# Optimization experiments

Hardware: AMD Instinct MI355X
Metric: run time of the kernel (lower is better)

## Reference

```python
import jax, jax.numpy as jnp
import numpy as np

N = 50000       # nodes
E = 1_600_000   # edges
F_IN, H1, H2, T, C = 16, 64, 64, 8, 10


def setup_inputs() -> dict:
    key = jax.random.key(0)
    ks = jax.random.split(key, 12)
    def w(k, shp):
        fan_in = shp[0]
        return jax.random.normal(k, shp, dtype=jnp.float32) * (1.0 / np.sqrt(fan_in))
    return {
        "x": jax.random.normal(ks[0], (N, F_IN, T), dtype=jnp.float32),
        "edge_index": jax.random.randint(ks[1], (2, E), 0, N, dtype=jnp.int64),
        "edge_weight": jax.random.uniform(ks[2], (E,), dtype=jnp.float32),
        "W1": w(ks[3], (F_IN, H1)), "b1": jnp.zeros((H1,), jnp.float32),
        "W2": w(ks[4], (H1, H2)),   "b2": jnp.zeros((H2,), jnp.float32),
        "W3": w(ks[5], (H2, H2)),   "b3": jnp.zeros((H2,), jnp.float32),
        "Wseq": w(ks[6], (H2 * T, H2)), "bseq": jnp.zeros((H2,), jnp.float32),
        "Wcls": w(ks[7], (H2, C)),  "bcls": jnp.zeros((C,), jnp.float32),
    }


def reference(x, edge_index, edge_weight, W1, b1, W2, b2, W3, b3, Wseq, bseq, Wcls, bcls):
    n = x.shape[0]
    src, dst = edge_index[0], edge_index[1]
    # GCN: add self-loops with weight 1, symmetric degree normalization
    loops = jnp.arange(n, dtype=src.dtype)
    src_a = jnp.concatenate([src, loops])
    dst_a = jnp.concatenate([dst, loops])
    w_a = jnp.concatenate([edge_weight, jnp.ones((n,), edge_weight.dtype)])
    deg = jax.ops.segment_sum(w_a, dst_a, num_segments=n)
    dinv = jnp.where(deg > 0, jax.lax.rsqrt(jnp.where(deg > 0, deg, 1.0)), 0.0)
    norm = dinv[src_a] * w_a * dinv[dst_a]  # [E+N]

    def conv(h, W, b):
        h = h @ W                                  # [N, out]
        msg = h[src_a] * norm[:, None]             # gather + scale
        return jax.ops.segment_sum(msg, dst_a, num_segments=n) + b

    def per_t(xt):  # xt: [N, F_IN]
        h = jax.nn.relu(conv(xt, W1, b1))
        h = jax.nn.relu(conv(h, W2, b2))
        h = jax.nn.relu(conv(h, W3, b3))
        return h  # [N, H2]

    hs = jax.vmap(per_t)(jnp.moveaxis(x, -1, 0))   # [T, N, H2]
    seq = jnp.transpose(hs, (1, 0, 2)).reshape(n, -1)  # [N, T*H2], t-major like torch.cat
    h = jax.nn.relu(seq @ Wseq + bseq)
    return h @ Wcls + bcls  # [N, C]
```

## Files before the change

kernel.cpp:

```cpp
#include <hip/hip_runtime.h>
#include <hip/hip_fp16.h>

constexpr int N  = 50000;
constexpr int E  = 1600000;
constexpr int T  = 8;
constexpr int H  = 64;
constexpr int C  = 10;

__global__ void deg_count_kernel(const int* __restrict__ ei, const float* __restrict__ w,
                                 float* __restrict__ deg, int* __restrict__ counts) {
  int e = blockIdx.x * blockDim.x + threadIdx.x;
  if (e >= E) return;
  int d = ei[E + e];
  atomicAdd(&deg[d], w[e]);
  atomicAdd(&counts[d], 1);
}

__global__ void dinv_kernel(float* deg) {
  int n = blockIdx.x * blockDim.x + threadIdx.x;
  if (n >= N) return;
  deg[n] = rsqrtf(deg[n] + 1.0f);
}

__global__ void scanA_kernel(const int* __restrict__ counts, int* __restrict__ rowptr,
                             int* __restrict__ bsum) {
  __shared__ int ws[4];
  int b = blockIdx.x, t = threadIdx.x;
  int base = b * 1024 + t * 4;
  int v0 = (base + 0 < N) ? counts[base + 0] : 0;
  int v1 = (base + 1 < N) ? counts[base + 1] : 0;
  int v2 = (base + 2 < N) ? counts[base + 2] : 0;
  int v3 = (base + 3 < N) ? counts[base + 3] : 0;
  int s = v0 + v1 + v2 + v3;
  int lane = t & 63, wid = t >> 6;
  int x = s;
  #pragma unroll
  for (int off = 1; off < 64; off <<= 1) {
    int y = __shfl_up(x, off, 64);
    if (lane >= off) x += y;
  }
  if (lane == 63) ws[wid] = x;
  __syncthreads();
  int woff = 0;
  #pragma unroll
  for (int k = 0; k < 4; ++k) if (k < wid) woff += ws[k];
  int excl = x + woff - s;
  int a = excl;
  a += v0; if (base + 0 < N) rowptr[base + 1] = a;
  a += v1; if (base + 1 < N) rowptr[base + 2] = a;
  a += v2; if (base + 2 < N) rowptr[base + 3] = a;
  a += v3; if (base + 3 < N) rowptr[base + 4] = a;
  if (t == 255) bsum[b] = x + woff;
}

__global__ void scanB_kernel(const int* __restrict__ bsum, int* __restrict__ boff, int nb) {
  int t = threadIdx.x;
  int v = (t < nb) ? bsum[t] : 0;
  int x = v;
  #pragma unroll
  for (int off = 1; off < 64; off <<= 1) {
    int y = __shfl_up(x, off, 64);
    if (t >= off) x += y;
  }
  if (t < nb) boff[t] = x - v;
}

__global__ void scanC_kernel(int* __restrict__ rowptr, const int* __restrict__ boff) {
  int i = blockIdx.x * 256 + threadIdx.x;
  if (i == 0) rowptr[0] = 0;
  if (i < N) rowptr[i + 1] += boff[i >> 10];
}

__global__ void fill_kernel(const int* __restrict__ ei, const float* __restrict__ w,
                            const float* __restrict__ dinv, const int* __restrict__ rowptr,
                            int* __restrict__ fill, int* __restrict__ csr_src,
                            float* __restrict__ csr_norm) {
  int e = blockIdx.x * blockDim.x + threadIdx.x;
  if (e >= E) return;
  int s = ei[e], d = ei[E + e];
  int pos = rowptr[d] + atomicAdd(&fill[d], 1);
  csr_src[pos] = s;
  csr_norm[pos] = dinv[s] * w[e] * dinv[d];
}

__global__ void cvt_x_kernel(const float* __restrict__ x, __half* __restrict__ xh) {
  int i = blockIdx.x * blockDim.x + threadIdx.x;
  if (i >= N * 32) return;
  float4 v = ((const float4*)x)[i];
  __half2 h0; h0.x = __float2half_rn(v.x); h0.y = __float2half_rn(v.y);
  __half2 h1; h1.x = __float2half_rn(v.z); h1.y = __float2half_rn(v.w);
  uint2 u;
  u.x = __builtin_bit_cast(unsigned int, h0);
  u.y = __builtin_bit_cast(unsigned int, h1);
  ((uint2*)xh)[i] = u;
}

__device__ __forceinline__ void accum8(float* acc, uint4 r, float wgt) {
  float2 f0 = __half22float2(__builtin_bit_cast(__half2, r.x));
  float2 f1 = __half22float2(__builtin_bit_cast(__half2, r.y));
  float2 f2 = __half22float2(__builtin_bit_cast(__half2, r.z));
  float2 f3 = __half22float2(__builtin_bit_cast(__half2, r.w));
  acc[0] = fmaf(wgt, f0.x, acc[0]); acc[1] = fmaf(wgt, f0.y, acc[1]);
  acc[2] = fmaf(wgt, f1.x, acc[2]); acc[3] = fmaf(wgt, f1.y, acc[3]);
  acc[4] = fmaf(wgt, f2.x, acc[4]); acc[5] = fmaf(wgt, f2.y, acc[5]);
  acc[6] = fmaf(wgt, f3.x, acc[6]); acc[7] = fmaf(wgt, f3.y, acc[7]);
}

__global__ void agg_x_kernel(const __half* __restrict__ xh, const float* __restrict__ dinv,
                             const int* __restrict__ rowptr, const int* __restrict__ csr_src,
                             const float* __restrict__ csr_norm, float* __restrict__ xagg) {
  int tid = threadIdx.x;
  int w = tid >> 6, l = tid & 63;
  int sub = l >> 4, q = l & 15;
  int n = blockIdx.x * 4 + w;
  float di = dinv[n], dd = di * di;
  int e0 = rowptr[n], e1 = rowptr[n + 1];
  int cnt = e1 - e0 + 1;
  float acc[8] = {0, 0, 0, 0, 0, 0, 0, 0};
  int sA, sB; float wA, wB;
  auto meta = [&](int idx, int& s_, float& w_) {
    if (idx == 0)       { s_ = n; w_ = dd; }
    else if (idx < cnt) { s_ = csr_src[e0 + idx - 1]; w_ = csr_norm[e0 + idx - 1]; }
    else                { s_ = n; w_ = 0.f; }
  };
  meta(sub,     sA, wA);
  meta(sub + 4, sB, wB);
  for (int i = sub; i < cnt; i += 8) {
    uint4 rA = *reinterpret_cast<const uint4*>(xh + (size_t)sA * 128 + q * 8);
    uint4 rB = *reinterpret_cast<const uint4*>(xh + (size_t)sB * 128 + q * 8);
    float uA = wA, uB = wB;
    meta(i + 8,  sA, wA);
    meta(i + 12, sB, wB);
    accum8(acc, rA, uA);
    accum8(acc, rB, uB);
  }
  #pragma unroll
  for (int v = 0; v < 8; ++v) {
    acc[v] += __shfl_xor(acc[v], 16, 64);
    acc[v] += __shfl_xor(acc[v], 32, 64);
  }
  if (sub == 0) {
    float4 o0; o0.x = acc[0]; o0.y = acc[1]; o0.z = acc[2]; o0.w = acc[3];
    float4 o1; o1.x = acc[4]; o1.y = acc[5]; o1.z = acc[6]; o1.w = acc[7];
    float4* dst = (float4*)(xagg + (size_t)n * 128 + q * 8);
    dst[0] = o0; dst[1] = o1;
  }
}

__global__ void dense12_kernel(const float* __restrict__ xagg, const float* __restrict__ W1,
                               const float* __restrict__ b1, const float* __restrict__ W2,
                               __half* __restrict__ G2h) {
  __shared__ float xs[4 * 128];
  __shared__ float h1s[4][8][64];
  int tid = threadIdx.x;
  int n0 = blockIdx.x * 4;
  ((float2*)xs)[tid] = ((const float2*)(xagg + (size_t)n0 * 128))[tid];
  __syncthreads();
  int nb = tid >> 6, j = tid & 63;
  float a[8];
  float bj = b1[j];
  #pragma unroll
  for (int t = 0; t < 8; ++t) a[t] = bj;
  for (int f = 0; f < 16; ++f) {
    float wv = W1[f * 64 + j];
    #pragma unroll
    for (int t = 0; t < 8; ++t) a[t] = fmaf(xs[nb * 128 + f * 8 + t], wv, a[t]);
  }
  #pragma unroll
  for (int t = 0; t < 8; ++t) h1s[nb][t][j] = fmaxf(a[t], 0.f);
  __syncthreads();
  float g[8];
  #pragma unroll
  for (int t = 0; t < 8; ++t) g[t] = 0.f;
  for (int k = 0; k < 64; ++k) {
    float wv = W2[k * 64 + j];
    #pragma unroll
    for (int t = 0; t < 8; ++t) g[t] = fmaf(h1s[nb][t][k], wv, g[t]);
  }
  __half* gp = G2h + (size_t)(n0 + nb) * 512 + j;
  #pragma unroll
  for (int t = 0; t < 8; ++t) gp[t * 64] = __float2half_rn(g[t]);
}

__global__ void conv2w_kernel(const __half* __restrict__ G2h, const float* __restrict__ dinv,
                              const int* __restrict__ rowptr, const int* __restrict__ csr_src,
                              const float* __restrict__ csr_norm, const float* __restrict__ b2,
                              const float* __restrict__ W3, __half* __restrict__ G3h) {
  __shared__ float h2s[4][512];
  int tid = threadIdx.x;
  int w = tid >> 6, l = tid & 63;
  int n0 = blockIdx.x * 4;
  int n = n0 + w;
  float di = dinv[n], dd = di * di;
  int e0 = rowptr[n], e1 = rowptr[n + 1];
  int cnt = e1 - e0 + 1;
  float acc[8] = {0, 0, 0, 0, 0, 0, 0, 0};
  int sm[4]; float wm[4];
  #pragma unroll
  for (int q = 0; q < 4; ++q) {
    int idx = q;
    if (idx == 0)       { sm[q] = n; wm[q] = dd; }
    else if (idx < cnt) { int e = e0 + idx - 1; sm[q] = csr_src[e]; wm[q] = csr_norm[e]; }
    else                { sm[q] = n; wm[q] = 0.f; }
  }
  for (int i = 0; i < cnt; i += 4) {
    uint4 r0 = *reinterpret_cast<const uint4*>(G2h + (size_t)sm[0] * 512 + l * 8);
    uint4 r1 = *reinterpret_cast<const uint4*>(G2h + (size_t)sm[1] * 512 + l * 8);
    uint4 r2 = *reinterpret_cast<const uint4*>(G2h + (size_t)sm[2] * 512 + l * 8);
    uint4 r3 = *reinterpret_cast<const uint4*>(G2h + (size_t)sm[3] * 512 + l * 8);
    float w0 = wm[0], w1 = wm[1], w2 = wm[2], w3 = wm[3];
    #pragma unroll
    for (int q = 0; q < 4; ++q) {
      int idx = i + 4 + q;
      if (idx < cnt) { int e = e0 + idx - 1; sm[q] = csr_src[e]; wm[q] = csr_norm[e]; }
      else           { sm[q] = n; wm[q] = 0.f; }
    }
    accum8(acc, r0, w0);
    accum8(acc, r1, w1);
    accum8(acc, r2, w2);
    accum8(acc, r3, w3);
  }
  #pragma unroll
  for (int q = 0; q < 8; ++q)
    h2s[w][l * 8 + q] = fmaxf(acc[q] + b2[(l * 8 + q) & 63], 0.f);
  __syncthreads();
  int t = tid >> 5;
  int jh = tid & 31, j0 = 2 * jh;
  float g[4][2];
  #pragma unroll
  for (int q = 0; q < 4; ++q) { g[q][0] = 0.f; g[q][1] = 0.f; }
  const float2* W3v = (const float2*)W3;
  for (int k = 0; k < 64; ++k) {
    float2 wv = W3v[k * 32 + jh];
    #pragma unroll
    for (int q = 0; q < 4; ++q) {
      float h = h2s[q][t * 64 + k];
      g[q][0] = fmaf(h, wv.x, g[q][0]);
      g[q][1] = fmaf(h, wv.y, g[q][1]);
    }
  }
  #pragma unroll
  for (int q = 0; q < 4; ++q) {
    __half2 hv;
    hv.x = __float2half_rn(g[q][0]);
    hv.y = __float2half_rn(g[q][1]);
    *reinterpret_cast<__half2*>(G3h + (size_t)(n0 + q) * 512 + t * 64 + j0) = hv;
  }
}

__global__ void conv3w_kernel(const __half* __restrict__ G3h, const float* __restrict__ dinv,
                              const int* __restrict__ rowptr, const int* __restrict__ csr_src,
                              const float* __restrict__ csr_norm, const float* __restrict__ b3,
                              const float* __restrict__ Wseq, const float* __restrict__ bseq,
                              const float* __restrict__ Wcls, const float* __restrict__ bcls,
                              float* __restrict__ out) {
  __shared__ float h3s[4][512];
  __shared__ float red[4][4][64];
  __shared__ float hfs[4][64];
  int tid = threadIdx.x;
  int w = tid >> 6, l = tid & 63;
  int n0 = blockIdx.x * 4;
  int n = n0 + w;
  float di = dinv[n], dd = di * di;
  int e0 = rowptr[n], e1 = rowptr[n + 1];
  int cnt = e1 - e0 + 1;
  float acc[8] = {0, 0, 0, 0, 0, 0, 0, 0};
  int sm[4]; float wm[4];
  #pragma unroll
  for (int q = 0; q < 4; ++q) {
    int idx = q;
    if (idx == 0)       { sm[q] = n; wm[q] = dd; }
    else if (idx < cnt) { int e = e0 + idx - 1; sm[q] = csr_src[e]; wm[q] = csr_norm[e]; }
    else                { sm[q] = n; wm[q] = 0.f; }
  }
  for (int i = 0; i < cnt; i += 4) {
    uint4 r0 = *reinterpret_cast<const uint4*>(G3h + (size_t)sm[0] * 512 + l * 8);
    uint4 r1 = *reinterpret_cast<const uint4*>(G3h + (size_t)sm[1] * 512 + l * 8);
    uint4 r2 = *reinterpret_cast<const uint4*>(G3h + (size_t)sm[2] * 512 + l * 8);
    uint4 r3 = *reinterpret_cast<const uint4*>(G3h + (size_t)sm[3] * 512 + l * 8);
    float w0 = wm[0], w1 = wm[1], w2 = wm[2], w3 = wm[3];
    #pragma unroll
    for (int q = 0; q < 4; ++q) {
      int idx = i + 4 + q;
      if (idx < cnt) { int e = e0 + idx - 1; sm[q] = csr_src[e]; wm[q] = csr_norm[e]; }
      else           { sm[q] = n; wm[q] = 0.f; }
    }
    accum8(acc, r0, w0);
    accum8(acc, r1, w1);
    accum8(acc, r2, w2);
    accum8(acc, r3, w3);
  }
  #pragma unroll
  for (int q = 0; q < 8; ++q)
    h3s[w][l * 8 + q] = fmaxf(acc[q] + b3[(l * 8 + q) & 63], 0.f);
  __syncthreads();
  int p = tid >> 6, j = tid & 63;
  float pa0 = 0.f, pa1 = 0.f, pa2 = 0.f, pa3 = 0.f;
  for (int ci = 0; ci < 128; ++ci) {
    int c = p * 128 + ci;
    float wv = Wseq[(size_t)c * 64 + j];
    pa0 = fmaf(h3s[0][c], wv, pa0);
    pa1 = fmaf(h3s[1][c], wv, pa1);
    pa2 = fmaf(h3s[2][c], wv, pa2);
    pa3 = fmaf(h3s[3][c], wv, pa3);
  }
  red[p][0][j] = pa0; red[p][1][j] = pa1; red[p][2][j] = pa2; red[p][3][j] = pa3;
  __syncthreads();
  int nb = tid >> 6, k = tid & 63;
  float s = red[0][nb][k] + red[1][nb][k] + red[2][nb][k] + red[3][nb][k] + bseq[k];
  hfs[nb][k] = fmaxf(s, 0.f);
  __syncthreads();
  if (k < C) {
    float o = bcls[k];
    #pragma unroll
    for (int kk = 0; kk < 64; ++kk) o = fmaf(hfs[nb][kk], Wcls[kk * C + k], o);
    out[(size_t)(n0 + nb) * C + k] = o;
  }
}

__global__ void layer1N_kernel(const float* __restrict__ xagg, const float* __restrict__ W1,
                               const float* __restrict__ b1, const float* __restrict__ W2,
                               float* __restrict__ GA, int t) {
  __shared__ float hs[4][H];
  int tid = threadIdx.x;
  int wv = tid >> 6, j = tid & 63;
  int n = blockIdx.x * 4 + wv;
  const float* xa = xagg + (size_t)n * 128;
  float a = b1[j];
  #pragma unroll
  for (int f = 0; f < 16; ++f) a += xa[f * 8 + t] * W1[f * H + j];
  hs[wv][j] = fmaxf(a, 0.f);
  __syncthreads();
  float g = 0.f;
  #pragma unroll
  for (int k = 0; k < H; ++k) g += hs[wv][k] * W2[k * H + j];
  GA[(size_t)n * H + j] = g;
}

template<bool ACCUM>
__global__ void convN_kernel(const float* __restrict__ Gin, const float* __restrict__ dinv,
                             const int* __restrict__ rowptr, const int* __restrict__ csr_src,
                             const float* __restrict__ csr_norm, const float* __restrict__ b,
                             const float* __restrict__ Wnext, float* __restrict__ Gout) {
  __shared__ __align__(16) float hs[4][H];
  int tid = threadIdx.x;
  int wv = tid >> 6, lane = tid & 63;
  int sub = lane >> 4, q = lane & 15;
  int n = blockIdx.x * 4 + wv;
  float di = dinv[n];
  const float4* G4 = (const float4*)Gin;
  float4 a0 = {0,0,0,0}, a1 = {0,0,0,0};
  int e0 = rowptr[n], e1 = rowptr[n + 1];
  int e = e0 + sub;
  for (; e + 4 < e1; e += 8) {
    int s0 = csr_src[e];     float w0 = csr_norm[e];
    int s1 = csr_src[e + 4]; float w1 = csr_norm[e + 4];
    float4 r0 = G4[(size_t)s0 * 16 + q];
    float4 r1 = G4[(size_t)s1 * 16 + q];
    a0.x += w0 * r0.x; a0.y += w0 * r0.y; a0.z += w0 * r0.z; a0.w += w0 * r0.w;
    a1.x += w1 * r1.x; a1.y += w1 * r1.y; a1.z += w1 * r1.z; a1.w += w1 * r1.w;
  }
  for (; e < e1; e += 4) {
    int s0 = csr_src[e]; float w0 = csr_norm[e];
    float4 r0 = G4[(size_t)s0 * 16 + q];
    a0.x += w0 * r0.x; a0.y += w0 * r0.y; a0.z += w0 * r0.z; a0.w += w0 * r0.w;
  }
  a0.x += a1.x; a0.y += a1.y; a0.z += a1.z; a0.w += a1.w;
  #pragma unroll
  for (int off = 16; off <= 32; off <<= 1) {
    a0.x += __shfl_xor(a0.x, off, 64);
    a0.y += __shfl_xor(a0.y, off, 64);
    a0.z += __shfl_xor(a0.z, off, 64);
    a0.w += __shfl_xor(a0.w, off, 64);
  }
  float4 own = G4[(size_t)n * 16 + q];
  float dd = di * di;
  if (sub == 0) {
    float4 h;
    h.x = fmaxf(a0.x + dd * own.x + b[4 * q + 0], 0.f);
    h.y = fmaxf(a0.y + dd * own.y + b[4 * q + 1], 0.f);
    h.z = fmaxf(a0.z + dd * own.z + b[4 * q + 2], 0.f);
    h.w = fmaxf(a0.w + dd * own.w + b[4 * q + 3], 0.f);
    ((float4*)hs[wv])[q] = h;
  }
  __syncthreads();
  float g = 0.f;
  #pragma unroll
  for (int k = 0; k < H; ++k) g += hs[wv][k] * Wnext[k * H + lane];
  if (ACCUM) Gout[(size_t)n * H + lane] += g;
  else       Gout[(size_t)n * H + lane]  = g;
}

__global__ void final_kernel(const float* __restrict__ acc, const float* __restrict__ bseq,
                             const float* __restrict__ Wcls, const float* __restrict__ bcls,
                             float* __restrict__ out) {
  __shared__ float hs[4][H];
  int tid = threadIdx.x;
  int wv = tid >> 6, j = tid & 63;
  int n = blockIdx.x * 4 + wv;
  hs[wv][j] = fmaxf(acc[(size_t)n * H + j] + bseq[j], 0.0f);
  __syncthreads();
  if (j < C) {
    float o = bcls[j];
    #pragma unroll
    for (int k = 0; k < H; ++k) o += hs[wv][k] * Wcls[k * C + j];
    out[(size_t)n * C + j] = o;
  }
}

extern "C" void kernel_launch(void* const* d_in, const int* in_sizes, int n_in,
                              void* d_out, int out_size, void* d_ws, size_t ws_size,
                              hipStream_t stream) {
  const float* x    = (const float*)d_in[0];
  const int*   ei   = (const int*)  d_in[1];
  const float* w    = (const float*)d_in[2];
  const float* W1   = (const float*)d_in[3];
  const float* b1   = (const float*)d_in[4];
  const float* W2   = (const float*)d_in[5];
  const float* b2   = (const float*)d_in[6];
  const float* W3   = (const float*)d_in[7];
  const float* b3   = (const float*)d_in[8];
  const float* Wseq = (const float*)d_in[9];
  const float* bseq = (const float*)d_in[10];
  const float* Wcls = (const float*)d_in[11];
  const float* bcls = (const float*)d_in[12];
  float* out = (float*)d_out;

  char* p = (char*)d_ws;
  auto alloc = [&](size_t bytes) -> char* {
    char* r = p; p += (bytes + 255) & ~(size_t)255; return r;
  };
  float*  deg     = (float*) alloc((size_t)N * 4);
  int*    counts  = (int*)   alloc((size_t)N * 4);
  int*    fillc   = (int*)   alloc((size_t)N * 4);
  int*    rowptr  = (int*)   alloc((size_t)(N + 1) * 4);
  int*    bsum    = (int*)   alloc(64 * 4);
  int*    boff    = (int*)   alloc(64 * 4);
  int*    csr_src = (int*)   alloc((size_t)E * 4);
  float*  csr_nrm = (float*) alloc((size_t)E * 4);
  float*  xagg    = (float*) alloc((size_t)N * 128 * 4);
  __half* xh      = (__half*)alloc((size_t)N * 128 * 2);

  hipMemsetAsync(deg,    0, (size_t)N * 4, stream);
  hipMemsetAsync(counts, 0, (size_t)N * 4, stream);
  hipMemsetAsync(fillc,  0, (size_t)N * 4, stream);

  constexpr int NTILES = (N + 1023) / 1024;
  cvt_x_kernel<<<(N * 32 + 255) / 256, 256, 0, stream>>>(x, xh);
  deg_count_kernel<<<(E + 255) / 256, 256, 0, stream>>>(ei, w, deg, counts);
  dinv_kernel<<<(N + 255) / 256, 256, 0, stream>>>(deg);
  scanA_kernel<<<NTILES, 256, 0, stream>>>(counts, rowptr, bsum);
  scanB_kernel<<<1, 64, 0, stream>>>(bsum, boff, NTILES);
  scanC_kernel<<<(N + 255) / 256, 256, 0, stream>>>(rowptr, boff);
  fill_kernel<<<(E + 255) / 256, 256, 0, stream>>>(ei, w, deg, rowptr, fillc, csr_src, csr_nrm);
  agg_x_kernel<<<N / 4, 256, 0, stream>>>(xh, deg, rowptr, csr_src, csr_nrm, xagg);

  bool wide = ws_size >= (size_t)155 * 1000 * 1000;

  if (wide) {
    __half* G2h = (__half*)alloc((size_t)N * 512 * 2);
    __half* G3h = (__half*)alloc((size_t)N * 512 * 2);
    dense12_kernel<<<N / 4, 256, 0, stream>>>(xagg, W1, b1, W2, G2h);
    conv2w_kernel<<<N / 4, 256, 0, stream>>>(G2h, deg, rowptr, csr_src, csr_nrm, b2, W3, G3h);
    conv3w_kernel<<<N / 4, 256, 0, stream>>>(G3h, deg, rowptr, csr_src, csr_nrm, b3,
                                             Wseq, bseq, Wcls, bcls, out);
  } else {
    float* GA  = (float*)alloc((size_t)N * H * 4);
    float* GB  = (float*)alloc((size_t)N * H * 4);
    float* acc = (float*)alloc((size_t)N * H * 4);
    hipMemsetAsync(acc, 0, (size_t)N * H * 4, stream);
    for (int t = 0; t < T; ++t) {
      layer1N_kernel<<<N / 4, 256, 0, stream>>>(xagg, W1, b1, W2, GA, t);
      convN_kernel<false><<<N / 4, 256, 0, stream>>>(GA, deg, rowptr, csr_src, csr_nrm, b2, W3, GB);
      convN_kernel<true ><<<N / 4, 256, 0, stream>>>(GB, deg, rowptr, csr_src, csr_nrm, b3,
                                                     Wseq + (size_t)t * H * H, acc);
    }
    final_kernel<<<N / 4, 256, 0, stream>>>(acc, bseq, Wcls, bcls, out);
  }
}
```

Before: 836.2 us.

## Pad CSR rows to multiples of eight with self-loop and store norms in fp16

Builds the CSR with the self-loop entry folded in at each row start and rows padded to a multiple of eight using zero-weight dummy entries, so the gather loops run without index branches or self-loop special cases. Edge norms are stored as half precision, halving that metadata traffic. A new kernel writes the self and pad entries. The cost is up to seven extra gathered rows per node and reduced precision on the normalisation weights.

```diff
diff --git a/kernel.cpp b/kernel.cpp
--- a/kernel.cpp
+++ b/kernel.cpp
@@ -6,6 +6,7 @@
 constexpr int T  = 8;
 constexpr int H  = 64;
 constexpr int C  = 10;
+constexpr int CSR_CAP = E + 8 * N + 64;
 
 __global__ void deg_count_kernel(const int* __restrict__ ei, const float* __restrict__ w,
                                  float* __restrict__ deg, int* __restrict__ counts) {
@@ -27,10 +28,11 @@
   __shared__ int ws[4];
   int b = blockIdx.x, t = threadIdx.x;
   int base = b * 1024 + t * 4;
-  int v0 = (base + 0 < N) ? counts[base + 0] : 0;
-  int v1 = (base + 1 < N) ? counts[base + 1] : 0;
-  int v2 = (base + 2 < N) ? counts[base + 2] : 0;
-  int v3 = (base + 3 < N) ? counts[base + 3] : 0;
+  auto pad8 = [](int c) { return (c + 8) & ~7; };
+  int v0 = (base + 0 < N) ? pad8(counts[base + 0]) : 0;
+  int v1 = (base + 1 < N) ? pad8(counts[base + 1]) : 0;
+  int v2 = (base + 2 < N) ? pad8(counts[base + 2]) : 0;
+  int v3 = (base + 3 < N) ? pad8(counts[base + 3]) : 0;
   int s = v0 + v1 + v2 + v3;
   int lane = t & 63, wid = t >> 6;
   int x = s;
@@ -44,8 +46,7 @@
   int woff = 0;
   #pragma unroll
   for (int k = 0; k < 4; ++k) if (k < wid) woff += ws[k];
-  int excl = x + woff - s;
-  int a = excl;
+  int a = x + woff - s;
   a += v0; if (base + 0 < N) rowptr[base + 1] = a;
   a += v1; if (base + 1 < N) rowptr[base + 2] = a;
   a += v2; if (base + 2 < N) rowptr[base + 3] = a;
@@ -71,16 +72,31 @@
   if (i < N) rowptr[i + 1] += boff[i >> 10];
 }
 
+__global__ void self_pad_kernel(const int* __restrict__ counts, const int* __restrict__ rowptr,
+                                const float* __restrict__ dinv, int* __restrict__ csr_src,
+                                __half* __restrict__ csr_nrmh) {
+  int n = blockIdx.x * 256 + threadIdx.x;
+  if (n >= N) return;
+  int base = rowptr[n], end = rowptr[n + 1];
+  float di = dinv[n];
+  csr_src[base] = n;
+  csr_nrmh[base] = __float2half_rn(di * di);
+  for (int i = base + 1 + counts[n]; i < end; ++i) {
+    csr_src[i] = n;
+    csr_nrmh[i] = __float2half_rn(0.f);
+  }
+}
+
 __global__ void fill_kernel(const int* __restrict__ ei, const float* __restrict__ w,
                             const float* __restrict__ dinv, const int* __restrict__ rowptr,
                             int* __restrict__ fill, int* __restrict__ csr_src,
-                            float* __restrict__ csr_norm) {
+                            __half* __restrict__ csr_nrmh) {
   int e = blockIdx.x * blockDim.x + threadIdx.x;
   if (e >= E) return;
   int s = ei[e], d = ei[E + e];
-  int pos = rowptr[d] + atomicAdd(&fill[d], 1);
+  int pos = rowptr[d] + 1 + atomicAdd(&fill[d], 1);
   csr_src[pos] = s;
-  csr_norm[pos] = dinv[s] * w[e] * dinv[d];
+  csr_nrmh[pos] = __float2half_rn(dinv[s] * w[e] * dinv[d]);
 }
 
 __global__ void cvt_x_kernel(const float* __restrict__ x, __half* __restrict__ xh) {
@@ -106,31 +122,25 @@
   acc[6] = fmaf(wgt, f3.x, acc[6]); acc[7] = fmaf(wgt, f3.y, acc[7]);
 }
 
-__global__ void agg_x_kernel(const __half* __restrict__ xh, const float* __restrict__ dinv,
-                             const int* __restrict__ rowptr, const int* __restrict__ csr_src,
-                             const float* __restrict__ csr_norm, float* __restrict__ xagg) {
+__global__ void agg_x_kernel(const __half* __restrict__ xh, const int* __restrict__ rowptr,
+                             const int* __restrict__ csr_src, const __half* __restrict__ csr_nrmh,
+                             float* __restrict__ xagg) {
   int tid = threadIdx.x;
   int w = tid >> 6, l = tid & 63;
   int sub = l >> 4, q = l & 15;
   int n = blockIdx.x * 4 + w;
-  float di = dinv[n], dd = di * di;
-  int e0 = rowptr[n], e1 = rowptr[n + 1];
-  int cnt = e1 - e0 + 1;
+  int e0 = rowptr[n], cnt = rowptr[n + 1] - e0;
   float acc[8] = {0, 0, 0, 0, 0, 0, 0, 0};
-  int sA, sB; float wA, wB;
-  auto meta = [&](int idx, int& s_, float& w_) {
-    if (idx == 0)       { s_ = n; w_ = dd; }
-    else if (idx < cnt) { s_ = csr_src[e0 + idx - 1]; w_ = csr_norm[e0 + idx - 1]; }
-    else                { s_ = n; w_ = 0.f; }
-  };
-  meta(sub,     sA, wA);
-  meta(sub + 4, sB, wB);
+  int   sA = csr_src[e0 + sub],      sB = csr_src[e0 + sub + 4];
+  float wA = __half2float(csr_nrmh[e0 + sub]);
+  float wB = __half2float(csr_nrmh[e0 + sub + 4]);
   for (int i = sub; i < cnt; i += 8) {
     uint4 rA = *reinterpret_cast<const uint4*>(xh + (size_t)sA * 128 + q * 8);
     uint4 rB = *reinterpret_cast<const uint4*>(xh + (size_t)sB * 128 + q * 8);
     float uA = wA, uB = wB;
-    meta(i + 8,  sA, wA);
-    meta(i + 12, sB, wB);
+    int j = e0 + i + 8;
+    sA = csr_src[j];     wA = __half2float(csr_nrmh[j]);
+    sB = csr_src[j + 4]; wB = __half2float(csr_nrmh[j + 4]);
     accum8(acc, rA, uA);
     accum8(acc, rB, uB);
   }
@@ -182,26 +192,22 @@
   for (int t = 0; t < 8; ++t) gp[t * 64] = __float2half_rn(g[t]);
 }
 
-__global__ void conv2w_kernel(const __half* __restrict__ G2h, const float* __restrict__ dinv,
-                              const int* __restrict__ rowptr, const int* __restrict__ csr_src,
-                              const float* __restrict__ csr_norm, const float* __restrict__ b2,
+__global__ void conv2w_kernel(const __half* __restrict__ G2h, const int* __restrict__ rowptr,
+                              const int* __restrict__ csr_src, const __half* __restrict__ csr_nrmh,
+                              const float* __restrict__ b2,
                               const float* __restrict__ W3, __half* __restrict__ G3h) {
   __shared__ float h2s[4][512];
   int tid = threadIdx.x;
   int w = tid >> 6, l = tid & 63;
   int n0 = blockIdx.x * 4;
   int n = n0 + w;
-  float di = dinv[n], dd = di * di;
-  int e0 = rowptr[n], e1 = rowptr[n + 1];
-  int cnt = e1 - e0 + 1;
+  int e0 = rowptr[n], cnt = rowptr[n + 1] - e0;
   float acc[8] = {0, 0, 0, 0, 0, 0, 0, 0};
   int sm[4]; float wm[4];
   #pragma unroll
   for (int q = 0; q < 4; ++q) {
-    int idx = q;
-    if (idx == 0)       { sm[q] = n; wm[q] = dd; }
-    else if (idx < cnt) { int e = e0 + idx - 1; sm[q] = csr_src[e]; wm[q] = csr_norm[e]; }
-    else                { sm[q] = n; wm[q] = 0.f; }
+    sm[q] = csr_src[e0 + q];
+    wm[q] = __half2float(csr_nrmh[e0 + q]);
   }
   for (int i = 0; i < cnt; i += 4) {
     uint4 r0 = *reinterpret_cast<const uint4*>(G2h + (size_t)sm[0] * 512 + l * 8);
@@ -211,9 +217,9 @@
     float w0 = wm[0], w1 = wm[1], w2 = wm[2], w3 = wm[3];
     #pragma unroll
     for (int q = 0; q < 4; ++q) {
-      int idx = i + 4 + q;
-      if (idx < cnt) { int e = e0 + idx - 1; sm[q] = csr_src[e]; wm[q] = csr_norm[e]; }
-      else           { sm[q] = n; wm[q] = 0.f; }
+      int j = e0 + i + 4 + q;
+      sm[q] = csr_src[j];
+      wm[q] = __half2float(csr_nrmh[j]);
     }
     accum8(acc, r0, w0);
     accum8(acc, r1, w1);
@@ -248,9 +254,9 @@
   }
 }
 
-__global__ void conv3w_kernel(const __half* __restrict__ G3h, const float* __restrict__ dinv,
-                              const int* __restrict__ rowptr, const int* __restrict__ csr_src,
-                              const float* __restrict__ csr_norm, const float* __restrict__ b3,
+__global__ void conv3w_kernel(const __half* __restrict__ G3h, const int* __restrict__ rowptr,
+                              const int* __restrict__ csr_src, const __half* __restrict__ csr_nrmh,
+                              const float* __restrict__ b3,
                               const float* __restrict__ Wseq, const float* __restrict__ bseq,
                               const float* __restrict__ Wcls, const float* __restrict__ bcls,
                               float* __restrict__ out) {
@@ -261,17 +267,13 @@
   int w = tid >> 6, l = tid & 63;
   int n0 = blockIdx.x * 4;
   int n = n0 + w;
-  float di = dinv[n], dd = di * di;
-  int e0 = rowptr[n], e1 = rowptr[n + 1];
-  int cnt = e1 - e0 + 1;
+  int e0 = rowptr[n], cnt = rowptr[n + 1] - e0;
   float acc[8] = {0, 0, 0, 0, 0, 0, 0, 0};
   int sm[4]; float wm[4];
   #pragma unroll
   for (int q = 0; q < 4; ++q) {
-    int idx = q;
-    if (idx == 0)       { sm[q] = n; wm[q] = dd; }
-    else if (idx < cnt) { int e = e0 + idx - 1; sm[q] = csr_src[e]; wm[q] = csr_norm[e]; }
-    else                { sm[q] = n; wm[q] = 0.f; }
+    sm[q] = csr_src[e0 + q];
+    wm[q] = __half2float(csr_nrmh[e0 + q]);
   }
   for (int i = 0; i < cnt; i += 4) {
     uint4 r0 = *reinterpret_cast<const uint4*>(G3h + (size_t)sm[0] * 512 + l * 8);
@@ -281,9 +283,9 @@
     float w0 = wm[0], w1 = wm[1], w2 = wm[2], w3 = wm[3];
     #pragma unroll
     for (int q = 0; q < 4; ++q) {
-      int idx = i + 4 + q;
-      if (idx < cnt) { int e = e0 + idx - 1; sm[q] = csr_src[e]; wm[q] = csr_norm[e]; }
-      else           { sm[q] = n; wm[q] = 0.f; }
+      int j = e0 + i + 4 + q;
+      sm[q] = csr_src[j];
+      wm[q] = __half2float(csr_nrmh[j]);
     }
     accum8(acc, r0, w0);
     accum8(acc, r1, w1);
@@ -338,34 +340,24 @@
 }
 
 template<bool ACCUM>
-__global__ void convN_kernel(const float* __restrict__ Gin, const float* __restrict__ dinv,
-                             const int* __restrict__ rowptr, const int* __restrict__ csr_src,
-                             const float* __restrict__ csr_norm, const float* __restrict__ b,
+__global__ void convN_kernel(const float* __restrict__ Gin, const int* __restrict__ rowptr,
+                             const int* __restrict__ csr_src, const __half* __restrict__ csr_nrmh,
+                             const float* __restrict__ b,
                              const float* __restrict__ Wnext, float* __restrict__ Gout) {
   __shared__ __align__(16) float hs[4][H];
   int tid = threadIdx.x;
   int wv = tid >> 6, lane = tid & 63;
   int sub = lane >> 4, q = lane & 15;
   int n = blockIdx.x * 4 + wv;
-  float di = dinv[n];
   const float4* G4 = (const float4*)Gin;
-  float4 a0 = {0,0,0,0}, a1 = {0,0,0,0};
+  float4 a0 = {0,0,0,0};
   int e0 = rowptr[n], e1 = rowptr[n + 1];
-  int e = e0 + sub;
-  for (; e + 4 < e1; e += 8) {
-    int s0 = csr_src[e];     float w0 = csr_norm[e];
-    int s1 = csr_src[e + 4]; float w1 = csr_norm[e + 4];
-    float4 r0 = G4[(size_t)s0 * 16 + q];
-    float4 r1 = G4[(size_t)s1 * 16 + q];
-    a0.x += w0 * r0.x; a0.y += w0 * r0.y; a0.z += w0 * r0.z; a0.w += w0 * r0.w;
-    a1.x += w1 * r1.x; a1.y += w1 * r1.y; a1.z += w1 * r1.z; a1.w += w1 * r1.w;
-  }
-  for (; e < e1; e += 4) {
-    int s0 = csr_src[e]; float w0 = csr_norm[e];
+  for (int e = e0 + sub; e < e1; e += 4) {
+    int s0 = csr_src[e];
+    float w0 = __half2float(csr_nrmh[e]);
     float4 r0 = G4[(size_t)s0 * 16 + q];
     a0.x += w0 * r0.x; a0.y += w0 * r0.y; a0.z += w0 * r0.z; a0.w += w0 * r0.w;
   }
-  a0.x += a1.x; a0.y += a1.y; a0.z += a1.z; a0.w += a1.w;
   #pragma unroll
   for (int off = 16; off <= 32; off <<= 1) {
     a0.x += __shfl_xor(a0.x, off, 64);
@@ -373,14 +365,12 @@
     a0.z += __shfl_xor(a0.z, off, 64);
     a0.w += __shfl_xor(a0.w, off, 64);
   }
-  float4 own = G4[(size_t)n * 16 + q];
-  float dd = di * di;
   if (sub == 0) {
     float4 h;
-    h.x = fmaxf(a0.x + dd * own.x + b[4 * q + 0], 0.f);
-    h.y = fmaxf(a0.y + dd * own.y + b[4 * q + 1], 0.f);
-    h.z = fmaxf(a0.z + dd * own.z + b[4 * q + 2], 0.f);
-    h.w = fmaxf(a0.w + dd * own.w + b[4 * q + 3], 0.f);
+    h.x = fmaxf(a0.x + b[4 * q + 0], 0.f);
+    h.y = fmaxf(a0.y + b[4 * q + 1], 0.f);
+    h.z = fmaxf(a0.z + b[4 * q + 2], 0.f);
+    h.w = fmaxf(a0.w + b[4 * q + 3], 0.f);
     ((float4*)hs[wv])[q] = h;
   }
   __syncthreads();
@@ -436,8 +426,8 @@
   int*    rowptr  = (int*)   alloc((size_t)(N + 1) * 4);
   int*    bsum    = (int*)   alloc(64 * 4);
   int*    boff    = (int*)   alloc(64 * 4);
-  int*    csr_src = (int*)   alloc((size_t)E * 4);
-  float*  csr_nrm = (float*) alloc((size_t)E * 4);
+  int*    csr_src = (int*)   alloc((size_t)CSR_CAP * 4);
+  __half* csr_nrmh= (__half*)alloc((size_t)CSR_CAP * 2);
   float*  xagg    = (float*) alloc((size_t)N * 128 * 4);
   __half* xh      = (__half*)alloc((size_t)N * 128 * 2);
 
@@ -452,8 +442,9 @@
   scanA_kernel<<<NTILES, 256, 0, stream>>>(counts, rowptr, bsum);
   scanB_kernel<<<1, 64, 0, stream>>>(bsum, boff, NTILES);
   scanC_kernel<<<(N + 255) / 256, 256, 0, stream>>>(rowptr, boff);
-  fill_kernel<<<(E + 255) / 256, 256, 0, stream>>>(ei, w, deg, rowptr, fillc, csr_src, csr_nrm);
-  agg_x_kernel<<<N / 4, 256, 0, stream>>>(xh, deg, rowptr, csr_src, csr_nrm, xagg);
+  self_pad_kernel<<<(N + 255) / 256, 256, 0, stream>>>(counts, rowptr, deg, csr_src, csr_nrmh);
+  fill_kernel<<<(E + 255) / 256, 256, 0, stream>>>(ei, w, deg, rowptr, fillc, csr_src, csr_nrmh);
+  agg_x_kernel<<<N / 4, 256, 0, stream>>>(xh, rowptr, csr_src, csr_nrmh, xagg);
 
   bool wide = ws_size >= (size_t)155 * 1000 * 1000;
 
@@ -461,8 +452,8 @@
     __half* G2h = (__half*)alloc((size_t)N * 512 * 2);
     __half* G3h = (__half*)alloc((size_t)N * 512 * 2);
     dense12_kernel<<<N / 4, 256, 0, stream>>>(xagg, W1, b1, W2, G2h);
-    conv2w_kernel<<<N / 4, 256, 0, stream>>>(G2h, deg, rowptr, csr_src, csr_nrm, b2, W3, G3h);
-    conv3w_kernel<<<N / 4, 256, 0, stream>>>(G3h, deg, rowptr, csr_src, csr_nrm, b3,
+    conv2w_kernel<<<N / 4, 256, 0, stream>>>(G2h, rowptr, csr_src, csr_nrmh, b2, W3, G3h);
+    conv3w_kernel<<<N / 4, 256, 0, stream>>>(G3h, rowptr, csr_src, csr_nrmh, b3,
                                              Wseq, bseq, Wcls, bcls, out);
   } else {
     float* GA  = (float*)alloc((size_t)N * H * 4);
@@ -471,8 +462,8 @@
     hipMemsetAsync(acc, 0, (size_t)N * H * 4, stream);
     for (int t = 0; t < T; ++t) {
       layer1N_kernel<<<N / 4, 256, 0, stream>>>(xagg, W1, b1, W2, GA, t);
-      convN_kernel<false><<<N / 4, 256, 0, stream>>>(GA, deg, rowptr, csr_src, csr_nrm, b2, W3, GB);
-      convN_kernel<true ><<<N / 4, 256, 0, stream>>>(GB, deg, rowptr, csr_src, csr_nrm, b3,
+      convN_kernel<false><<<N / 4, 256, 0, stream>>>(GA, rowptr, csr_src, csr_nrmh, b2, W3, GB);
+      convN_kernel<true ><<<N / 4, 256, 0, stream>>>(GB, rowptr, csr_src, csr_nrmh, b3,
                                                      Wseq + (size_t)t * H * H, acc);
     }
     final_kernel<<<N / 4, 256, 0, stream>>>(acc, bseq, Wcls, bcls, out);
```

Result: slower. 861.8 us (+3.1%).
